# Performance work log

Measured on AMD Instinct MI355X. Metric: run time of the kernel, lower is better.

The kernel has to match this reference:

```python
import jax, jax.numpy as jnp
import numpy as np


def setup_inputs() -> dict:
    key = jax.random.key(0)
    ks = jax.random.split(key, 4)
    B, S, D, NH, H = 8, 1024, 1024, 16, 64
    x = jax.random.normal(ks[0], (B, S, D), dtype=jnp.float32)
    # xavier_normal_ for [NH, D, H]: std = sqrt(2/(D+H))
    weight = jax.random.normal(ks[1], (NH, D, H), dtype=jnp.float32) * np.sqrt(2.0 / (D + H))
    # nn.Linear default init ~ U(-1/sqrt(fan_in), 1/sqrt(fan_in))
    bound = 1.0 / np.sqrt(NH * H)
    lin_w = jax.random.uniform(ks[2], (D, NH * H), dtype=jnp.float32, minval=-bound, maxval=bound)
    lin_b = jax.random.uniform(ks[3], (D,), dtype=jnp.float32, minval=-bound, maxval=bound)
    ln_g = jnp.ones((D,), dtype=jnp.float32)
    ln_b = jnp.zeros((D,), dtype=jnp.float32)
    return {"x": x, "weight": weight, "lin_w": lin_w, "lin_b": lin_b, "ln_g": ln_g, "ln_b": ln_b}


def reference(x, weight, lin_w, lin_b, ln_g, ln_b):
    B, S, D = x.shape
    NH, _, H = weight.shape
    scale = 1.0 / np.sqrt(H)
    # per-head projection: [NH, B, S, H]
    logits = jnp.einsum('bsd,ndh->nbsh', x, weight)
    # self-attention scores (Q = K = V = logits): [NH, B, S, S]
    attn = jax.nn.softmax(jnp.einsum('nbsh,nbth->nbst', logits, logits) * scale, axis=-1)
    out = jnp.einsum('nbst,nbth->nbsh', attn, logits)      # [NH, B, S, H]
    # head concat along features: [B, S, NH*H]
    out = out.transpose(1, 2, 0, 3).reshape(B, S, NH * H)
    out = out @ lin_w.T + lin_b                             # [B, S, D]
    # dropout is identity in eval mode
    y = x + out
    mu = jnp.mean(y, axis=-1, keepdims=True)
    var = jnp.mean((y - mu) ** 2, axis=-1, keepdims=True)
    y = (y - mu) * jax.lax.rsqrt(var + 1e-5) * ln_g + ln_b
    # torch returns attn of shape [NH*B, S, S] (head-major)
    return y, attn.reshape(NH * B, S, S)
```

## Files before the change

### kernel.cpp

```cpp
#include <hip/hip_runtime.h>

typedef __bf16 bf16_t;
typedef __bf16 bf16x8 __attribute__((ext_vector_type(8)));
typedef float floatx4 __attribute__((ext_vector_type(4)));

#define GLD_LDS16(g, l) \
    __builtin_amdgcn_global_load_lds((const __attribute__((address_space(1))) void*)(g), \
                                     (__attribute__((address_space(3))) void*)(l), 16, 0, 0)

__global__ __launch_bounds__(256) void cvt_x(const float* __restrict__ x,
                                             bf16_t* __restrict__ xb) {
    int i = (blockIdx.x * 256 + threadIdx.x) * 4;
    float4 v = *(const float4*)&x[i];
    bf16_t* o = &xb[i];
    o[0] = (bf16_t)v.x; o[1] = (bf16_t)v.y; o[2] = (bf16_t)v.z; o[3] = (bf16_t)v.w;
}

__global__ __launch_bounds__(256) void prep_w(const float* __restrict__ w,
                                              bf16_t* __restrict__ wt) {
    int o = blockIdx.x * 256 + threadIdx.x;
    int d = o & 1023, nh = o >> 10;
    int n = nh >> 6, h = nh & 63;
    wt[o] = (bf16_t)w[(size_t)n * 65536 + (size_t)d * 64 + h];
}

__global__ __launch_bounds__(256) void cvt_linw(const float* __restrict__ lw,
                                                bf16_t* __restrict__ lb) {
    int i = (blockIdx.x * 256 + threadIdx.x) * 4;
    float4 v = *(const float4*)&lw[i];
    bf16_t* o = &lb[i];
    o[0] = (bf16_t)v.x; o[1] = (bf16_t)v.y; o[2] = (bf16_t)v.z; o[3] = (bf16_t)v.w;
}

__global__ __launch_bounds__(256) void gemm_ad(const bf16_t* __restrict__ A,
                                               const bf16_t* __restrict__ Bt,
                                               int mode,
                                               bf16_t* __restrict__ out_bf,
                                               float* __restrict__ out_f,
                                               const float* __restrict__ bias,
                                               const float* __restrict__ xres) {
    __shared__ __attribute__((aligned(16))) bf16_t As[128][64];
    __shared__ __attribute__((aligned(16))) bf16_t Bs[128][64];
    int tid = threadIdx.x;
    int bm = blockIdx.x * 128, bn = blockIdx.y * 128;
    int wave = tid >> 6, lane = tid & 63;
    int wm = (wave >> 1) * 64, wn = (wave & 1) * 64;
    int l15 = lane & 15, quad = lane >> 4;
    floatx4 acc[4][4] = {};
    int srow = lane >> 3;
    int scol = 8 * ((lane & 7) ^ srow);
    const bf16_t* abase = A  + (size_t)bm * 1024;
    const bf16_t* bbase = Bt + (size_t)bn * 1024;
    for (int kt = 0; kt < 1024; kt += 64) {
        __syncthreads();
        for (int i = 0; i < 4; i++) {
            int seg = wave * 4 + i;
            int r = seg * 8 + srow;
            GLD_LDS16(abase + (size_t)r * 1024 + kt + scol, (char*)&As[0][0] + seg * 1024);
            GLD_LDS16(bbase + (size_t)r * 1024 + kt + scol, (char*)&Bs[0][0] + seg * 1024);
        }
        __syncthreads();
        for (int ks = 0; ks < 2; ks++) {
            bf16x8 af[4], bfr[4];
            for (int mi = 0; mi < 4; mi++) {
                int row = wm + mi * 16 + l15;
                int cb = (ks * 64 + quad * 16) ^ ((row & 7) << 4);
                af[mi] = *(const bf16x8*)((const char*)&As[row][0] + cb);
            }
            for (int ni = 0; ni < 4; ni++) {
                int row = wn + ni * 16 + l15;
                int cb = (ks * 64 + quad * 16) ^ ((row & 7) << 4);
                bfr[ni] = *(const bf16x8*)((const char*)&Bs[row][0] + cb);
            }
            for (int mi = 0; mi < 4; mi++)
                for (int ni = 0; ni < 4; ni++)
                    acc[mi][ni] = __builtin_amdgcn_mfma_f32_16x16x32_bf16(af[mi], bfr[ni], acc[mi][ni], 0, 0, 0);
        }
    }
    for (int mi = 0; mi < 4; mi++)
        for (int ni = 0; ni < 4; ni++) {
            int col = bn + wn + ni * 16 + l15;
            for (int r = 0; r < 4; r++) {
                int row = bm + wm + mi * 16 + quad * 4 + r;
                size_t idx = (size_t)row * 1024 + col;
                float v = acc[mi][ni][r];
                if (mode == 0) out_bf[idx] = (bf16_t)v;
                else           out_f[idx] = v + bias[col] + xres[idx];
            }
        }
}

__global__ __launch_bounds__(256) void transpose_v(const bf16_t* __restrict__ logits,
                                                   bf16_t* __restrict__ vt) {
    __shared__ __attribute__((aligned(16))) bf16_t T[64][72];
    int nb = blockIdx.y;
    int n = nb >> 3, b = nb & 7;
    int s0 = blockIdx.x * 64;
    int tid = threadIdx.x;
    const bf16_t* src = logits + (size_t)(b * 1024 + s0) * 1024 + n * 64;
    for (int i = 0; i < 2; i++) {
        int c = tid + i * 256;
        int r = c >> 3, c8 = (c & 7) * 8;
        *(bf16x8*)&T[r][c8] = *(const bf16x8*)&src[(size_t)r * 1024 + c8];
    }
    __syncthreads();
    bf16_t* dst = vt + (size_t)nb * 64 * 1024 + s0;
    for (int i = 0; i < 2; i++) {
        int c = tid + i * 256;
        int h = c >> 3, sx = (c & 7) * 8;
        bf16x8 o;
        for (int j = 0; j < 8; j++) o[j] = T[sx + j][h];
        *(bf16x8*)&dst[(size_t)h * 1024 + sx] = o;
    }
}

__global__ __launch_bounds__(256) void fused_attn(const bf16_t* __restrict__ logits,
                                                  const bf16_t* __restrict__ vt,
                                                  float* __restrict__ attn,
                                                  bf16_t* __restrict__ outh) {
    __shared__ __attribute__((aligned(16))) bf16_t Qs[64][72];
    __shared__ __attribute__((aligned(16))) bf16_t Ks[128][72];
    __shared__ __attribute__((aligned(16))) bf16_t Vts[64][136];
    __shared__ __attribute__((aligned(16))) bf16_t Pl[4][16][136];
    int nb = blockIdx.y;
    int n = nb >> 3, b = nb & 7;
    int r0 = blockIdx.x * 64;
    int tid = threadIdx.x;
    int wave = tid >> 6, lane = tid & 63;
    int l15 = lane & 15, quad = lane >> 4;
    const bf16_t* qbase = logits + (size_t)(b * 1024 + r0) * 1024 + n * 64;
    const bf16_t* kbase = logits + (size_t)(b * 1024) * 1024 + n * 64;
    const bf16_t* vbase = vt + (size_t)nb * 64 * 1024;

    for (int i = 0; i < 2; i++) {
        int c = tid + i * 256;
        int r = c >> 3, c8 = (c & 7) * 8;
        *(bf16x8*)&Qs[r][c8] = *(const bf16x8*)&qbase[(size_t)r * 1024 + c8];
    }

    float rsum[4] = {0.f, 0.f, 0.f, 0.f};
    for (int t0 = 0; t0 < 1024; t0 += 128) {
        __syncthreads();
        for (int i = 0; i < 4; i++) {
            int c = tid + i * 256;
            int r = c >> 3, c8 = (c & 7) * 8;
            *(bf16x8*)&Ks[r][c8] = *(const bf16x8*)&kbase[(size_t)(t0 + r) * 1024 + c8];
        }
        __syncthreads();
        floatx4 acc[8] = {};
        for (int ks = 0; ks < 2; ks++) {
            bf16x8 a = *(const bf16x8*)&Qs[wave * 16 + l15][ks * 32 + quad * 8];
            for (int ni = 0; ni < 8; ni++) {
                bf16x8 bf = *(const bf16x8*)&Ks[ni * 16 + l15][ks * 32 + quad * 8];
                acc[ni] = __builtin_amdgcn_mfma_f32_16x16x32_bf16(a, bf, acc[ni], 0, 0, 0);
            }
        }
        for (int ni = 0; ni < 8; ni++)
            for (int r = 0; r < 4; r++)
                rsum[r] += __expf(acc[ni][r] * 0.125f);
    }
    for (int off = 1; off < 16; off <<= 1)
        for (int r = 0; r < 4; r++) rsum[r] += __shfl_xor(rsum[r], off);
    float inv[4];
    for (int r = 0; r < 4; r++) inv[r] = 1.0f / rsum[r];

    floatx4 accpv[4] = {};
    float* obase = attn + (size_t)nb * 1048576 + (size_t)r0 * 1024;
    for (int t0 = 0; t0 < 1024; t0 += 128) {
        __syncthreads();
        for (int i = 0; i < 4; i++) {
            int c = tid + i * 256;
            int r = c >> 3, c8 = (c & 7) * 8;
            *(bf16x8*)&Ks[r][c8] = *(const bf16x8*)&kbase[(size_t)(t0 + r) * 1024 + c8];
        }
        for (int i = 0; i < 4; i++) {
            int c = tid + i * 256;
            int h = c >> 4, c8 = (c & 15) * 8;
            *(bf16x8*)&Vts[h][c8] = *(const bf16x8*)&vbase[(size_t)h * 1024 + t0 + c8];
        }
        __syncthreads();
        floatx4 acc[8] = {};
        for (int ks = 0; ks < 2; ks++) {
            bf16x8 a = *(const bf16x8*)&Qs[wave * 16 + l15][ks * 32 + quad * 8];
            for (int ni = 0; ni < 8; ni++) {
                bf16x8 bf = *(const bf16x8*)&Ks[ni * 16 + l15][ks * 32 + quad * 8];
                acc[ni] = __builtin_amdgcn_mfma_f32_16x16x32_bf16(a, bf, acc[ni], 0, 0, 0);
            }
        }
        for (int ni = 0; ni < 8; ni++)
            for (int r = 0; r < 4; r++) {
                float p = __expf(acc[ni][r] * 0.125f) * inv[r];
                int sl = wave * 16 + quad * 4 + r;
                obase[(size_t)sl * 1024 + t0 + ni * 16 + l15] = p;
                Pl[wave][quad * 4 + r][ni * 16 + l15] = (bf16_t)p;
            }
        for (int ks2 = 0; ks2 < 4; ks2++) {
            bf16x8 pa = *(const bf16x8*)&Pl[wave][l15][ks2 * 32 + quad * 8];
            for (int ni = 0; ni < 4; ni++) {
                bf16x8 bv = *(const bf16x8*)&Vts[ni * 16 + l15][ks2 * 32 + quad * 8];
                accpv[ni] = __builtin_amdgcn_mfma_f32_16x16x32_bf16(pa, bv, accpv[ni], 0, 0, 0);
            }
        }
    }
    for (int ni = 0; ni < 4; ni++) {
        int h = ni * 16 + l15;
        for (int r = 0; r < 4; r++) {
            int s = r0 + wave * 16 + quad * 4 + r;
            outh[(size_t)(b * 1024 + s) * 1024 + n * 64 + h] = (bf16_t)accpv[ni][r];
        }
    }
}

__global__ __launch_bounds__(256) void ln_kernel(const float* __restrict__ z,
                                                 const float* __restrict__ g,
                                                 const float* __restrict__ beta,
                                                 float* __restrict__ y) {
    size_t row = blockIdx.x;
    const float* p = z + row * 1024;
    int tid = threadIdx.x;
    float4 v = *(const float4*)&p[tid * 4];
    float s1 = v.x + v.y + v.z + v.w;
    float s2 = v.x * v.x + v.y * v.y + v.z * v.z + v.w * v.w;
    for (int off = 32; off; off >>= 1) {
        s1 += __shfl_xor(s1, off);
        s2 += __shfl_xor(s2, off);
    }
    __shared__ float r1[4], r2[4];
    int wave = tid >> 6;
    if ((tid & 63) == 0) { r1[wave] = s1; r2[wave] = s2; }
    __syncthreads();
    s1 = r1[0] + r1[1] + r1[2] + r1[3];
    s2 = r2[0] + r2[1] + r2[2] + r2[3];
    float mu = s1 * (1.0f / 1024.0f);
    float var = s2 * (1.0f / 1024.0f) - mu * mu;
    float rstd = rsqrtf(var + 1e-5f);
    float4 gv = *(const float4*)&g[tid * 4];
    float4 bv = *(const float4*)&beta[tid * 4];
    float4 o;
    o.x = (v.x - mu) * rstd * gv.x + bv.x;
    o.y = (v.y - mu) * rstd * gv.y + bv.y;
    o.z = (v.z - mu) * rstd * gv.z + bv.z;
    o.w = (v.w - mu) * rstd * gv.w + bv.w;
    *(float4*)&y[row * 1024 + tid * 4] = o;
}

extern "C" void kernel_launch(void* const* d_in, const int* in_sizes, int n_in,
                              void* d_out, int out_size, void* d_ws, size_t ws_size,
                              hipStream_t stream) {
    const float* x     = (const float*)d_in[0];
    const float* w     = (const float*)d_in[1];
    const float* lw    = (const float*)d_in[2];
    const float* lb    = (const float*)d_in[3];
    const float* lg    = (const float*)d_in[4];
    const float* lbeta = (const float*)d_in[5];
    float* y    = (float*)d_out;
    float* attn = y + 8388608;

    char* ws = (char*)d_ws;
    bf16_t* xb     = (bf16_t*)(ws);
    bf16_t* outh   = (bf16_t*)(ws);
    bf16_t* wt     = (bf16_t*)(ws + 16777216);
    bf16_t* lwb    = (bf16_t*)(ws + 18874368);
    bf16_t* logits = (bf16_t*)(ws + 20971520);
    float*  z      = (float*)(ws + 20971520);
    bf16_t* vt     = (bf16_t*)(ws + 37748736);

    hipLaunchKernelGGL(cvt_x,        dim3(8192),       dim3(256), 0, stream, x, xb);
    hipLaunchKernelGGL(prep_w,       dim3(4096),       dim3(256), 0, stream, w, wt);
    hipLaunchKernelGGL(cvt_linw,     dim3(1024),       dim3(256), 0, stream, lw, lwb);
    hipLaunchKernelGGL(gemm_ad,      dim3(64, 8),      dim3(256), 0, stream,
                       xb, wt, 0, logits, (float*)nullptr, (const float*)nullptr, (const float*)nullptr);
    hipLaunchKernelGGL(transpose_v,  dim3(16, 128),    dim3(256), 0, stream, logits, vt);
    hipLaunchKernelGGL(fused_attn,   dim3(16, 128),    dim3(256), 0, stream, logits, vt, attn, outh);
    hipLaunchKernelGGL(gemm_ad,      dim3(64, 8),      dim3(256), 0, stream,
                       outh, lwb, 1, (bf16_t*)nullptr, z, lb, x);
    hipLaunchKernelGGL(ln_kernel,    dim3(8192),       dim3(256), 0, stream, z, lg, lbeta, y);
}
```

Before: 858.3 us.

## Prefetch K/V tiles into registers, keep Q in registers, tile-transpose weight prep

In the attention kernel, the next K and V tiles are loaded from global memory into registers while the current tile is being computed, so load latency overlaps with the MFMA work. Q fragments now live in registers instead of LDS, which cuts shared memory use, and a launch-bounds hint asks for 3 blocks per CU. The weight prep kernel becomes an LDS-tiled transpose with coalesced vector loads and stores in place of strided scalar gathers. In exchange, register pressure rises, and the occupancy hint could force spills.

```diff
diff --git a/kernel.cpp b/kernel.cpp
--- a/kernel.cpp
+++ b/kernel.cpp
@@ -18,10 +18,26 @@
 
 __global__ __launch_bounds__(256) void prep_w(const float* __restrict__ w,
                                               bf16_t* __restrict__ wt) {
-    int o = blockIdx.x * 256 + threadIdx.x;
-    int d = o & 1023, nh = o >> 10;
-    int n = nh >> 6, h = nh & 63;
-    wt[o] = (bf16_t)w[(size_t)n * 65536 + (size_t)d * 64 + h];
+    __shared__ bf16_t Tb[64][72];
+    int n = blockIdx.y, d0 = blockIdx.x * 64;
+    int tid = threadIdx.x;
+    const float* src = w + (size_t)n * 65536 + (size_t)d0 * 64;
+    for (int i = 0; i < 4; i++) {
+        int c = tid + i * 256;
+        int r = c >> 4, c4 = (c & 15) * 4;
+        float4 v = *(const float4*)&src[(size_t)r * 64 + c4];
+        Tb[r][c4 + 0] = (bf16_t)v.x; Tb[r][c4 + 1] = (bf16_t)v.y;
+        Tb[r][c4 + 2] = (bf16_t)v.z; Tb[r][c4 + 3] = (bf16_t)v.w;
+    }
+    __syncthreads();
+    bf16_t* dst = wt + (size_t)(n * 64) * 1024 + d0;
+    for (int i = 0; i < 2; i++) {
+        int c = tid + i * 256;
+        int h = c >> 3, dx = (c & 7) * 8;
+        bf16x8 o;
+        for (int j = 0; j < 8; j++) o[j] = Tb[dx + j][h];
+        *(bf16x8*)&dst[(size_t)h * 1024 + dx] = o;
+    }
 }
 
 __global__ __launch_bounds__(256) void cvt_linw(const float* __restrict__ lw,
@@ -114,11 +130,10 @@
     }
 }
 
-__global__ __launch_bounds__(256) void fused_attn(const bf16_t* __restrict__ logits,
-                                                  const bf16_t* __restrict__ vt,
-                                                  float* __restrict__ attn,
-                                                  bf16_t* __restrict__ outh) {
-    __shared__ __attribute__((aligned(16))) bf16_t Qs[64][72];
+__global__ __launch_bounds__(256, 3) void fused_attn(const bf16_t* __restrict__ logits,
+                                                     const bf16_t* __restrict__ vt,
+                                                     float* __restrict__ attn,
+                                                     bf16_t* __restrict__ outh) {
     __shared__ __attribute__((aligned(16))) bf16_t Ks[128][72];
     __shared__ __attribute__((aligned(16))) bf16_t Vts[64][136];
     __shared__ __attribute__((aligned(16))) bf16_t Pl[4][16][136];
@@ -128,36 +143,48 @@
     int tid = threadIdx.x;
     int wave = tid >> 6, lane = tid & 63;
     int l15 = lane & 15, quad = lane >> 4;
-    const bf16_t* qbase = logits + (size_t)(b * 1024 + r0) * 1024 + n * 64;
     const bf16_t* kbase = logits + (size_t)(b * 1024) * 1024 + n * 64;
     const bf16_t* vbase = vt + (size_t)nb * 64 * 1024;
 
-    for (int i = 0; i < 2; i++) {
-        int c = tid + i * 256;
-        int r = c >> 3, c8 = (c & 7) * 8;
-        *(bf16x8*)&Qs[r][c8] = *(const bf16x8*)&qbase[(size_t)r * 1024 + c8];
-    }
-
+    bf16x8 qf[2];
+    {
+        const bf16_t* qrow = logits + (size_t)(b * 1024 + r0 + wave * 16 + l15) * 1024 + n * 64;
+        qf[0] = *(const bf16x8*)&qrow[quad * 8];
+        qf[1] = *(const bf16x8*)&qrow[32 + quad * 8];
+    }
+
+    int kr[4], kc[4], vh[4], vc[4];
+    for (int i = 0; i < 4; i++) {
+        int c = tid + i * 256;
+        kr[i] = c >> 3;  kc[i] = (c & 7) * 8;
+        vh[i] = c >> 4;  vc[i] = (c & 15) * 8;
+    }
+
+    bf16x8 kreg[4], vreg[4];
+    for (int i = 0; i < 4; i++)
+        kreg[i] = *(const bf16x8*)&kbase[(size_t)kr[i] * 1024 + kc[i]];
     float rsum[4] = {0.f, 0.f, 0.f, 0.f};
     for (int t0 = 0; t0 < 1024; t0 += 128) {
         __syncthreads();
-        for (int i = 0; i < 4; i++) {
-            int c = tid + i * 256;
-            int r = c >> 3, c8 = (c & 7) * 8;
-            *(bf16x8*)&Ks[r][c8] = *(const bf16x8*)&kbase[(size_t)(t0 + r) * 1024 + c8];
-        }
+        for (int i = 0; i < 4; i++) *(bf16x8*)&Ks[kr[i]][kc[i]] = kreg[i];
+        if (t0 < 896)
+            for (int i = 0; i < 4; i++)
+                kreg[i] = *(const bf16x8*)&kbase[(size_t)(t0 + 128 + kr[i]) * 1024 + kc[i]];
         __syncthreads();
         floatx4 acc[8] = {};
         for (int ks = 0; ks < 2; ks++) {
-            bf16x8 a = *(const bf16x8*)&Qs[wave * 16 + l15][ks * 32 + quad * 8];
             for (int ni = 0; ni < 8; ni++) {
                 bf16x8 bf = *(const bf16x8*)&Ks[ni * 16 + l15][ks * 32 + quad * 8];
-                acc[ni] = __builtin_amdgcn_mfma_f32_16x16x32_bf16(a, bf, acc[ni], 0, 0, 0);
+                acc[ni] = __builtin_amdgcn_mfma_f32_16x16x32_bf16(qf[ks], bf, acc[ni], 0, 0, 0);
             }
         }
         for (int ni = 0; ni < 8; ni++)
             for (int r = 0; r < 4; r++)
                 rsum[r] += __expf(acc[ni][r] * 0.125f);
+    }
+    for (int i = 0; i < 4; i++) {
+        kreg[i] = *(const bf16x8*)&kbase[(size_t)kr[i] * 1024 + kc[i]];
+        vreg[i] = *(const bf16x8*)&vbase[(size_t)vh[i] * 1024 + vc[i]];
     }
     for (int off = 1; off < 16; off <<= 1)
         for (int r = 0; r < 4; r++) rsum[r] += __shfl_xor(rsum[r], off);
@@ -168,23 +195,19 @@
     float* obase = attn + (size_t)nb * 1048576 + (size_t)r0 * 1024;
     for (int t0 = 0; t0 < 1024; t0 += 128) {
         __syncthreads();
-        for (int i = 0; i < 4; i++) {
-            int c = tid + i * 256;
-            int r = c >> 3, c8 = (c & 7) * 8;
-            *(bf16x8*)&Ks[r][c8] = *(const bf16x8*)&kbase[(size_t)(t0 + r) * 1024 + c8];
-        }
-        for (int i = 0; i < 4; i++) {
-            int c = tid + i * 256;
-            int h = c >> 4, c8 = (c & 15) * 8;
-            *(bf16x8*)&Vts[h][c8] = *(const bf16x8*)&vbase[(size_t)h * 1024 + t0 + c8];
-        }
+        for (int i = 0; i < 4; i++) *(bf16x8*)&Ks[kr[i]][kc[i]] = kreg[i];
+        for (int i = 0; i < 4; i++) *(bf16x8*)&Vts[vh[i]][vc[i]] = vreg[i];
+        if (t0 < 896)
+            for (int i = 0; i < 4; i++) {
+                kreg[i] = *(const bf16x8*)&kbase[(size_t)(t0 + 128 + kr[i]) * 1024 + kc[i]];
+                vreg[i] = *(const bf16x8*)&vbase[(size_t)vh[i] * 1024 + t0 + 128 + vc[i]];
+            }
         __syncthreads();
         floatx4 acc[8] = {};
         for (int ks = 0; ks < 2; ks++) {
-            bf16x8 a = *(const bf16x8*)&Qs[wave * 16 + l15][ks * 32 + quad * 8];
             for (int ni = 0; ni < 8; ni++) {
                 bf16x8 bf = *(const bf16x8*)&Ks[ni * 16 + l15][ks * 32 + quad * 8];
-                acc[ni] = __builtin_amdgcn_mfma_f32_16x16x32_bf16(a, bf, acc[ni], 0, 0, 0);
+                acc[ni] = __builtin_amdgcn_mfma_f32_16x16x32_bf16(qf[ks], bf, acc[ni], 0, 0, 0);
             }
         }
         for (int ni = 0; ni < 8; ni++)
@@ -266,7 +289,7 @@
     bf16_t* vt     = (bf16_t*)(ws + 37748736);
 
     hipLaunchKernelGGL(cvt_x,        dim3(8192),       dim3(256), 0, stream, x, xb);
-    hipLaunchKernelGGL(prep_w,       dim3(4096),       dim3(256), 0, stream, w, wt);
+    hipLaunchKernelGGL(prep_w,       dim3(16, 16),     dim3(256), 0, stream, w, wt);
     hipLaunchKernelGGL(cvt_linw,     dim3(1024),       dim3(256), 0, stream, lw, lwb);
     hipLaunchKernelGGL(gemm_ad,      dim3(64, 8),      dim3(256), 0, stream,
                        xb, wt, 0, logits, (float*)nullptr, (const float*)nullptr, (const float*)nullptr);
```

Result: no change. 852.1 us (-0.7%).
